# Performance work log

Measured on AMD Instinct MI355X. Metric: run time of the kernel, lower is better.

Reference implementation:

```python
import jax, jax.numpy as jnp
import numpy as np

B, T, D_IN, EMB, H = 2, 2048, 1024, 1024, 16
HD = EMB // H  # head_dim = 64


def setup_inputs() -> dict:
    key = jax.random.key(0)
    ks = jax.random.split(key, 3)
    scale_qkv = 1.0 / np.sqrt(D_IN)
    scale_o = 1.0 / np.sqrt(EMB)
    return {
        "x": jax.random.normal(ks[0], (B, T, D_IN), dtype=jnp.float32),
        "W_qkv": jax.random.normal(ks[1], (D_IN, 3 * EMB), dtype=jnp.float32) * scale_qkv,
        "b_qkv": jnp.zeros((3 * EMB,), dtype=jnp.float32),
        "W_o": jax.random.normal(ks[2], (EMB, EMB), dtype=jnp.float32) * scale_o,
        "b_o": jnp.zeros((EMB,), dtype=jnp.float32),
    }


def reference(x, W_qkv, b_qkv, W_o, b_o):
    b, t, _ = x.shape
    qkv = x @ W_qkv + b_qkv                      # [B,T,3*EMB]
    # Match torch: reshape to (B,T,H,3*HD) -> permute -> chunk into q,k,v
    qkv = qkv.reshape(b, t, H, 3 * HD).transpose(0, 2, 1, 3)  # [B,H,T,3*HD]
    q, k, v = jnp.split(qkv, 3, axis=-1)         # each [B,H,T,HD]
    scale = 1.0 / jnp.sqrt(jnp.asarray(HD, dtype=q.dtype))
    scores = jnp.einsum("bhqd,bhkd->bhqk", q, k) * scale  # [B,H,T,T]
    attn = jax.nn.softmax(scores, axis=-1)
    values = jnp.einsum("bhqk,bhkd->bhqd", attn, v)       # [B,H,T,HD]
    values = values.transpose(0, 2, 1, 3).reshape(b, t, EMB)
    return values @ W_o + b_o
```

## Files before the change

kernel.cpp:

```cpp
#include <hip/hip_runtime.h>
#include <math.h>

typedef __bf16 bf16x8 __attribute__((ext_vector_type(8)));
typedef float f32x4 __attribute__((ext_vector_type(4)));

#define GPTR(p) ((const __attribute__((address_space(1))) void*)(p))
#define LPTR(p) ((__attribute__((address_space(3))) void*)(p))

#define QSCALE 0.18033688011112042f

__device__ __forceinline__ unsigned short f2bf(float f) {
  unsigned int u = __float_as_uint(f);
  u += 0x7FFFu + ((u >> 16) & 1u);
  return (unsigned short)(u >> 16);
}

__device__ __forceinline__ unsigned int pack_bf2(float lo, float hi) {
  return __builtin_amdgcn_perm(__float_as_uint(hi) + 0x8000u,
                               __float_as_uint(lo) + 0x8000u, 0x07060302u);
}

__device__ __forceinline__ float fast_exp2(float x) {
#if __has_builtin(__builtin_amdgcn_exp2f)
  return __builtin_amdgcn_exp2f(x);
#else
  return exp2f(x);
#endif
}

__device__ __forceinline__ f32x4 zero4() {
  f32x4 z; z[0] = 0.f; z[1] = 0.f; z[2] = 0.f; z[3] = 0.f; return z;
}

__device__ __forceinline__ void permlane_swap32(unsigned int& a, unsigned int& b) {
  asm("v_permlane32_swap_b32 %0, %1" : "+v"(a), "+v"(b));
}
__device__ __forceinline__ void permlane_swap16(unsigned int& a, unsigned int& b) {
  asm("v_permlane16_swap_b32 %0, %1" : "+v"(a), "+v"(b));
}

__global__ void conv_x_bf16(const float* __restrict__ in, unsigned short* __restrict__ out) {
  int i = (blockIdx.x * 256 + threadIdx.x) * 4;
  float4 v = *(const float4*)(in + i);
  ushort4 o;
  o.x = f2bf(v.x); o.y = f2bf(v.y); o.z = f2bf(v.z); o.w = f2bf(v.w);
  *(ushort4*)(out + i) = o;
}

__global__ void transpose_conv(const float* __restrict__ in, unsigned short* __restrict__ out,
                               int K, int N) {
  __shared__ float tile[64][65];
  int k0 = blockIdx.y * 64, n0 = blockIdx.x * 64;
  int t = threadIdx.x;
#pragma unroll
  for (int p = 0; p < 16; ++p) {
    int l = p * 256 + t; int r = l >> 6, c = l & 63;
    tile[r][c] = in[(size_t)(k0 + r) * N + n0 + c];
  }
  __syncthreads();
#pragma unroll
  for (int p = 0; p < 16; ++p) {
    int l = p * 256 + t; int r = l >> 6, c = l & 63;
    out[(size_t)(n0 + r) * K + k0 + c] = f2bf(tile[c][r]);
  }
}

__global__ __launch_bounds__(256) void gemm_qkv(
    const unsigned short* __restrict__ A, const unsigned short* __restrict__ Bt,
    const float* __restrict__ bias,
    unsigned short* __restrict__ Qd, unsigned short* __restrict__ Kd,
    unsigned short* __restrict__ Vtd) {
  __shared__ unsigned short As[128 * 32];
  __shared__ unsigned short Bs[128 * 32];
  const int tid = threadIdx.x, wave = tid >> 6, lane = tid & 63;
  const int quad = lane >> 4, l16 = lane & 15;
  const int wm = (wave >> 1) * 64, wn = (wave & 1) * 64;
  const int m0 = blockIdx.y * 128, n0 = blockIdx.x * 128;
  f32x4 acc[4][4];
#pragma unroll
  for (int i = 0; i < 4; ++i)
#pragma unroll
    for (int j = 0; j < 4; ++j) acc[i][j] = zero4();

  const int c = wave * 64 + lane;
  const int rA = c >> 2, o16 = (c & 3) * 8;

  for (int k0 = 0; k0 < 1024; k0 += 32) {
    __syncthreads();
    __builtin_amdgcn_global_load_lds(GPTR(A + (size_t)(m0 + rA) * 1024 + k0 + o16),
                                     LPTR(As + wave * 512), 16, 0, 0);
    __builtin_amdgcn_global_load_lds(GPTR(A + (size_t)(m0 + 64 + rA) * 1024 + k0 + o16),
                                     LPTR(As + 2048 + wave * 512), 16, 0, 0);
    __builtin_amdgcn_global_load_lds(GPTR(Bt + (size_t)(n0 + rA) * 1024 + k0 + o16),
                                     LPTR(Bs + wave * 512), 16, 0, 0);
    __builtin_amdgcn_global_load_lds(GPTR(Bt + (size_t)(n0 + 64 + rA) * 1024 + k0 + o16),
                                     LPTR(Bs + 2048 + wave * 512), 16, 0, 0);
    __syncthreads();
    bf16x8 af[4], bfr[4];
#pragma unroll
    for (int mt = 0; mt < 4; ++mt)
      af[mt] = *(const bf16x8*)(As + (wm + mt * 16 + l16) * 32 + quad * 8);
#pragma unroll
    for (int nt = 0; nt < 4; ++nt)
      bfr[nt] = *(const bf16x8*)(Bs + (wn + nt * 16 + l16) * 32 + quad * 8);
#pragma unroll
    for (int mt = 0; mt < 4; ++mt)
#pragma unroll
      for (int nt = 0; nt < 4; ++nt)
        acc[mt][nt] = __builtin_amdgcn_mfma_f32_16x16x32_bf16(af[mt], bfr[nt], acc[mt][nt], 0, 0, 0);
  }

#pragma unroll
  for (int mt = 0; mt < 4; ++mt) {
#pragma unroll
    for (int nt = 0; nt < 4; ++nt) {
      int m = m0 + wm + mt * 16 + quad * 4;
      int n = n0 + wn + nt * 16 + l16;
      float bv = bias[n];
      int h = n / 192, rem = n - h * 192;
      int which = rem >> 6, d = rem & 63;
      int b = m >> 11, t0 = m & 2047;
      size_t head = (size_t)(b * 16 + h);
      f32x4 a = acc[mt][nt];
      if (which == 0) {
        size_t base = (head * 2048 + t0) * 64 + d;
#pragma unroll
        for (int i = 0; i < 4; ++i)
          Qd[base + (size_t)i * 64] = f2bf((a[i] + bv) * QSCALE);
      } else if (which == 1) {
        size_t base = head * 131072 + (size_t)(t0 >> 6) * 4096;
#pragma unroll
        for (int i = 0; i < 4; ++i) {
          int tt = t0 + i;
          Kd[base + (tt & 63) * 64 + (((d >> 3) ^ (tt & 7)) << 3) + (d & 7)] = f2bf(a[i] + bv);
        }
      } else {
        size_t base = head * 131072 + (size_t)(t0 >> 6) * 4096;
        ushort4 o;
        o.x = f2bf(a[0] + bv); o.y = f2bf(a[1] + bv);
        o.z = f2bf(a[2] + bv); o.w = f2bf(a[3] + bv);
        *(ushort4*)(Vtd + base + d * 64 + (((((t0 & 63) >> 3)) ^ (d & 7)) << 3) + (t0 & 7)) = o;
      }
    }
  }
}

__global__ __launch_bounds__(256) void flash_attn(
    const unsigned short* __restrict__ Qg,
    const unsigned short* __restrict__ Kg,
    const unsigned short* __restrict__ Vg,
    unsigned short* __restrict__ att) {
  __shared__ unsigned short Ks[2][4096];
  __shared__ unsigned short Vs[2][4096];
  const int tid = threadIdx.x, wave = tid >> 6, lane = tid & 63;
  const int quad = lane >> 4, l16 = lane & 15;
  const int h7 = l16 & 7;
  const int bh = blockIdx.y;
  const int q0 = blockIdx.x * 128 + wave * 32;

  bf16x8 bq[2][2];
#pragma unroll
  for (int qg = 0; qg < 2; ++qg)
#pragma unroll
    for (int kh = 0; kh < 2; ++kh)
      bq[qg][kh] = *(const bf16x8*)(Qg + ((size_t)bh * 2048 + q0 + qg * 16 + l16) * 64 + kh * 32 + quad * 8);

  f32x4 o[2][4];
#pragma unroll
  for (int qg = 0; qg < 2; ++qg)
#pragma unroll
    for (int i = 0; i < 4; ++i) o[qg][i] = zero4();
  float l_run[2] = {0.f, 0.f};

  const unsigned short* Kt = Kg + (size_t)bh * 131072 + lane * 8;
  const unsigned short* Vt = Vg + (size_t)bh * 131072 + lane * 8;
  const int so0 = wave * 512, so1 = (4 + wave) * 512;

#define STAGE_KV(buf, tile)                                                              \
  do {                                                                                   \
    const unsigned short* Kb_ = Kt + (tile) * 4096;                                      \
    const unsigned short* Vb_ = Vt + (tile) * 4096;                                      \
    __builtin_amdgcn_global_load_lds(GPTR(Kb_ + so0), LPTR(&Ks[buf][so0]), 16, 0, 0);    \
    __builtin_amdgcn_global_load_lds(GPTR(Kb_ + so1), LPTR(&Ks[buf][so1]), 16, 0, 0);    \
    __builtin_amdgcn_global_load_lds(GPTR(Vb_ + so0), LPTR(&Vs[buf][so0]), 16, 0, 0);    \
    __builtin_amdgcn_global_load_lds(GPTR(Vb_ + so1), LPTR(&Vs[buf][so1]), 16, 0, 0);    \
  } while (0)

  STAGE_KV(0, 0);
  __syncthreads();

  int cur = 0;
  for (int tile = 0; tile < 32; ++tile) {
    if (tile < 31) STAGE_KV(cur ^ 1, tile + 1);

    f32x4 s[2][4];
#pragma unroll
    for (int qg = 0; qg < 2; ++qg)
#pragma unroll
      for (int kt = 0; kt < 4; ++kt) s[qg][kt] = zero4();
#pragma unroll
    for (int kt = 0; kt < 4; ++kt) {
#pragma unroll
      for (int kh = 0; kh < 2; ++kh) {
        bf16x8 a = *(const bf16x8*)(&Ks[cur][(kt * 16 + l16) * 64 + (((kh * 4 + quad) ^ h7) << 3)]);
        s[0][kt] = __builtin_amdgcn_mfma_f32_16x16x32_bf16(a, bq[0][kh], s[0][kt], 0, 0, 0);
        s[1][kt] = __builtin_amdgcn_mfma_f32_16x16x32_bf16(a, bq[1][kh], s[1][kt], 0, 0, 0);
      }
    }

    unsigned int pw[2][4][2];
#pragma unroll
    for (int qg = 0; qg < 2; ++qg) {
      float lsum = 0.f;
      float pv[4][4];
#pragma unroll
      for (int kt = 0; kt < 4; ++kt)
#pragma unroll
        for (int r = 0; r < 4; ++r) {
          float p = fast_exp2(s[qg][kt][r]);
          pv[kt][r] = p;
          lsum += p;
        }
#pragma unroll
      for (int kt = 0; kt < 4; ++kt) {
        pw[qg][kt][0] = pack_bf2(pv[kt][0], pv[kt][1]);
        pw[qg][kt][1] = pack_bf2(pv[kt][2], pv[kt][3]);
      }
      lsum += __shfl_xor(lsum, 16);
      lsum += __shfl_xor(lsum, 32);
      l_run[qg] += lsum;
    }

    bf16x8 pf[2][2];
#pragma unroll
    for (int qg = 0; qg < 2; ++qg) {
#pragma unroll
      for (int st = 0; st < 2; ++st) {
        unsigned int a0 = pw[qg][2 * st][0], b0 = pw[qg][2 * st + 1][0];
        unsigned int a1 = pw[qg][2 * st][1], b1 = pw[qg][2 * st + 1][1];
        permlane_swap32(a0, b0); permlane_swap16(a0, b0);
        permlane_swap32(a1, b1); permlane_swap16(a1, b1);
        union { unsigned int u[4]; bf16x8 v; } x;
        x.u[0] = a0; x.u[1] = a1; x.u[2] = b0; x.u[3] = b1;
        pf[qg][st] = x.v;
      }
    }

#pragma unroll
    for (int st = 0; st < 2; ++st) {
#pragma unroll
      for (int mt = 0; mt < 4; ++mt) {
        bf16x8 av = *(const bf16x8*)(&Vs[cur][(mt * 16 + l16) * 64 + (((st * 4 + quad) ^ h7) << 3)]);
        o[0][mt] = __builtin_amdgcn_mfma_f32_16x16x32_bf16(av, pf[0][st], o[0][mt], 0, 0, 0);
        o[1][mt] = __builtin_amdgcn_mfma_f32_16x16x32_bf16(av, pf[1][st], o[1][mt], 0, 0, 0);
      }
    }

    __syncthreads();
    cur ^= 1;
  }
#undef STAGE_KV

  int b = bh >> 4, h = bh & 15;
#pragma unroll
  for (int qg = 0; qg < 2; ++qg) {
    float inv_l = 1.f / l_run[qg];
    unsigned short* orow = att + ((size_t)b * 2048 + q0 + qg * 16 + l16) * 1024 + h * 64;
#pragma unroll
    for (int mt = 0; mt < 4; ++mt) {
      ushort4 ov;
      ov.x = f2bf(o[qg][mt][0] * inv_l);
      ov.y = f2bf(o[qg][mt][1] * inv_l);
      ov.z = f2bf(o[qg][mt][2] * inv_l);
      ov.w = f2bf(o[qg][mt][3] * inv_l);
      *(ushort4*)(orow + mt * 16 + quad * 4) = ov;
    }
  }
}

__global__ __launch_bounds__(256) void gemm_out(
    const unsigned short* __restrict__ A, const unsigned short* __restrict__ Bt,
    const float* __restrict__ bias, float* __restrict__ out) {
  __shared__ unsigned short As[128 * 32];
  __shared__ unsigned short Bs[64 * 32];
  const int tid = threadIdx.x, wave = tid >> 6, lane = tid & 63;
  const int quad = lane >> 4, l16 = lane & 15;
  const int wm = (wave >> 1) * 64, wn = (wave & 1) * 32;
  const int m0 = blockIdx.y * 128, n0 = blockIdx.x * 64;
  f32x4 acc[4][2];
#pragma unroll
  for (int i = 0; i < 4; ++i)
#pragma unroll
    for (int j = 0; j < 2; ++j) acc[i][j] = zero4();

  const int c = wave * 64 + lane;
  const int rA = c >> 2, o16 = (c & 3) * 8;

  for (int k0 = 0; k0 < 1024; k0 += 32) {
    __syncthreads();
    __builtin_amdgcn_global_load_lds(GPTR(A + (size_t)(m0 + rA) * 1024 + k0 + o16),
                                     LPTR(As + wave * 512), 16, 0, 0);
    __builtin_amdgcn_global_load_lds(GPTR(A + (size_t)(m0 + 64 + rA) * 1024 + k0 + o16),
                                     LPTR(As + 2048 + wave * 512), 16, 0, 0);
    __builtin_amdgcn_global_load_lds(GPTR(Bt + (size_t)(n0 + rA) * 1024 + k0 + o16),
                                     LPTR(Bs + wave * 512), 16, 0, 0);
    __syncthreads();
    bf16x8 af[4], bfr[2];
#pragma unroll
    for (int mt = 0; mt < 4; ++mt)
      af[mt] = *(const bf16x8*)(As + (wm + mt * 16 + l16) * 32 + quad * 8);
#pragma unroll
    for (int nt = 0; nt < 2; ++nt)
      bfr[nt] = *(const bf16x8*)(Bs + (wn + nt * 16 + l16) * 32 + quad * 8);
#pragma unroll
    for (int mt = 0; mt < 4; ++mt)
#pragma unroll
      for (int nt = 0; nt < 2; ++nt)
        acc[mt][nt] = __builtin_amdgcn_mfma_f32_16x16x32_bf16(af[mt], bfr[nt], acc[mt][nt], 0, 0, 0);
  }

#pragma unroll
  for (int mt = 0; mt < 4; ++mt) {
#pragma unroll
    for (int nt = 0; nt < 2; ++nt) {
      int m = m0 + wm + mt * 16 + quad * 4;
      int n = n0 + wn + nt * 16 + l16;
      float bv = bias[n];
      float* orow = out + (size_t)m * 1024 + n;
      orow[0]        = acc[mt][nt][0] + bv;
      orow[1024]     = acc[mt][nt][1] + bv;
      orow[2 * 1024] = acc[mt][nt][2] + bv;
      orow[3 * 1024] = acc[mt][nt][3] + bv;
    }
  }
}

extern "C" void kernel_launch(void* const* d_in, const int* in_sizes, int n_in,
                              void* d_out, int out_size, void* d_ws, size_t ws_size,
                              hipStream_t stream) {
  const float* x    = (const float*)d_in[0];
  const float* Wqkv = (const float*)d_in[1];
  const float* bqkv = (const float*)d_in[2];
  const float* Wo   = (const float*)d_in[3];
  const float* bo   = (const float*)d_in[4];
  float* out = (float*)d_out;

  unsigned short* xb    = (unsigned short*)d_ws;
  unsigned short* wqkvt = xb    + (size_t)4096 * 1024;
  unsigned short* wot   = wqkvt + (size_t)3072 * 1024;
  unsigned short* Qd    = wot   + (size_t)1024 * 1024;
  unsigned short* Kd    = Qd    + (size_t)32 * 2048 * 64;
  unsigned short* Vtd   = Kd    + (size_t)32 * 2048 * 64;
  unsigned short* attb  = Vtd   + (size_t)32 * 2048 * 64;

  conv_x_bf16<<<4096, 256, 0, stream>>>(x, xb);
  transpose_conv<<<dim3(48, 16), 256, 0, stream>>>(Wqkv, wqkvt, 1024, 3072);
  transpose_conv<<<dim3(16, 16), 256, 0, stream>>>(Wo, wot, 1024, 1024);
  gemm_qkv<<<dim3(24, 32), 256, 0, stream>>>(xb, wqkvt, bqkv, Qd, Kd, Vtd);
  flash_attn<<<dim3(16, 32), 256, 0, stream>>>(Qd, Kd, Vtd, attb);
  gemm_out<<<dim3(16, 32), 256, 0, stream>>>(attb, wot, bo, out);
}
```

Before: 213.1 us.

## Double-buffer LDS tiles in QKV and output projection GEMMs

Both projection GEMMs now use two LDS buffers, issuing the async global-to-LDS loads for the next K slice before running the MFMAs on the current slice. The loop needs one barrier per iteration instead of two. The aim is to hide global load latency behind matrix math. It doubles LDS use per block, which may lower occupancy. The compiler's waitcnt handling for the async loads decides how much overlap is actually achieved.

```diff
diff --git a/kernel.cpp b/kernel.cpp
--- a/kernel.cpp
+++ b/kernel.cpp
@@ -70,8 +70,8 @@
     const float* __restrict__ bias,
     unsigned short* __restrict__ Qd, unsigned short* __restrict__ Kd,
     unsigned short* __restrict__ Vtd) {
-  __shared__ unsigned short As[128 * 32];
-  __shared__ unsigned short Bs[128 * 32];
+  __shared__ unsigned short As[2][4096];
+  __shared__ unsigned short Bs[2][4096];
   const int tid = threadIdx.x, wave = tid >> 6, lane = tid & 63;
   const int quad = lane >> 4, l16 = lane & 15;
   const int wm = (wave >> 1) * 64, wn = (wave & 1) * 64;
@@ -85,30 +85,39 @@
   const int c = wave * 64 + lane;
   const int rA = c >> 2, o16 = (c & 3) * 8;
 
+#define STAGEQ(B, K0)                                                                      \
+  do {                                                                                     \
+    __builtin_amdgcn_global_load_lds(GPTR(A + (size_t)(m0 + rA) * 1024 + (K0) + o16),      \
+                                     LPTR(&As[B][wave * 512]), 16, 0, 0);                  \
+    __builtin_amdgcn_global_load_lds(GPTR(A + (size_t)(m0 + 64 + rA) * 1024 + (K0) + o16), \
+                                     LPTR(&As[B][2048 + wave * 512]), 16, 0, 0);           \
+    __builtin_amdgcn_global_load_lds(GPTR(Bt + (size_t)(n0 + rA) * 1024 + (K0) + o16),     \
+                                     LPTR(&Bs[B][wave * 512]), 16, 0, 0);                  \
+    __builtin_amdgcn_global_load_lds(GPTR(Bt + (size_t)(n0 + 64 + rA) * 1024 + (K0) + o16),\
+                                     LPTR(&Bs[B][2048 + wave * 512]), 16, 0, 0);           \
+  } while (0)
+
+  STAGEQ(0, 0);
+  __syncthreads();
+  int cur = 0;
   for (int k0 = 0; k0 < 1024; k0 += 32) {
-    __syncthreads();
-    __builtin_amdgcn_global_load_lds(GPTR(A + (size_t)(m0 + rA) * 1024 + k0 + o16),
-                                     LPTR(As + wave * 512), 16, 0, 0);
-    __builtin_amdgcn_global_load_lds(GPTR(A + (size_t)(m0 + 64 + rA) * 1024 + k0 + o16),
-                                     LPTR(As + 2048 + wave * 512), 16, 0, 0);
-    __builtin_amdgcn_global_load_lds(GPTR(Bt + (size_t)(n0 + rA) * 1024 + k0 + o16),
-                                     LPTR(Bs + wave * 512), 16, 0, 0);
-    __builtin_amdgcn_global_load_lds(GPTR(Bt + (size_t)(n0 + 64 + rA) * 1024 + k0 + o16),
-                                     LPTR(Bs + 2048 + wave * 512), 16, 0, 0);
-    __syncthreads();
+    if (k0 < 992) STAGEQ(cur ^ 1, k0 + 32);
     bf16x8 af[4], bfr[4];
 #pragma unroll
     for (int mt = 0; mt < 4; ++mt)
-      af[mt] = *(const bf16x8*)(As + (wm + mt * 16 + l16) * 32 + quad * 8);
+      af[mt] = *(const bf16x8*)(&As[cur][(wm + mt * 16 + l16) * 32 + quad * 8]);
 #pragma unroll
     for (int nt = 0; nt < 4; ++nt)
-      bfr[nt] = *(const bf16x8*)(Bs + (wn + nt * 16 + l16) * 32 + quad * 8);
+      bfr[nt] = *(const bf16x8*)(&Bs[cur][(wn + nt * 16 + l16) * 32 + quad * 8]);
 #pragma unroll
     for (int mt = 0; mt < 4; ++mt)
 #pragma unroll
       for (int nt = 0; nt < 4; ++nt)
         acc[mt][nt] = __builtin_amdgcn_mfma_f32_16x16x32_bf16(af[mt], bfr[nt], acc[mt][nt], 0, 0, 0);
-  }
+    __syncthreads();
+    cur ^= 1;
+  }
+#undef STAGEQ
 
 #pragma unroll
   for (int mt = 0; mt < 4; ++mt) {
@@ -281,8 +290,8 @@
 __global__ __launch_bounds__(256) void gemm_out(
     const unsigned short* __restrict__ A, const unsigned short* __restrict__ Bt,
     const float* __restrict__ bias, float* __restrict__ out) {
-  __shared__ unsigned short As[128 * 32];
-  __shared__ unsigned short Bs[64 * 32];
+  __shared__ unsigned short As[2][4096];
+  __shared__ unsigned short Bs[2][2048];
   const int tid = threadIdx.x, wave = tid >> 6, lane = tid & 63;
   const int quad = lane >> 4, l16 = lane & 15;
   const int wm = (wave >> 1) * 64, wn = (wave & 1) * 32;
@@ -296,28 +305,37 @@
   const int c = wave * 64 + lane;
   const int rA = c >> 2, o16 = (c & 3) * 8;
 
+#define STAGEO(B, K0)                                                                      \
+  do {                                                                                     \
+    __builtin_amdgcn_global_load_lds(GPTR(A + (size_t)(m0 + rA) * 1024 + (K0) + o16),      \
+                                     LPTR(&As[B][wave * 512]), 16, 0, 0);                  \
+    __builtin_amdgcn_global_load_lds(GPTR(A + (size_t)(m0 + 64 + rA) * 1024 + (K0) + o16), \
+                                     LPTR(&As[B][2048 + wave * 512]), 16, 0, 0);           \
+    __builtin_amdgcn_global_load_lds(GPTR(Bt + (size_t)(n0 + rA) * 1024 + (K0) + o16),     \
+                                     LPTR(&Bs[B][wave * 512]), 16, 0, 0);                  \
+  } while (0)
+
+  STAGEO(0, 0);
+  __syncthreads();
+  int cur = 0;
   for (int k0 = 0; k0 < 1024; k0 += 32) {
-    __syncthreads();
-    __builtin_amdgcn_global_load_lds(GPTR(A + (size_t)(m0 + rA) * 1024 + k0 + o16),
-                                     LPTR(As + wave * 512), 16, 0, 0);
-    __builtin_amdgcn_global_load_lds(GPTR(A + (size_t)(m0 + 64 + rA) * 1024 + k0 + o16),
-                                     LPTR(As + 2048 + wave * 512), 16, 0, 0);
-    __builtin_amdgcn_global_load_lds(GPTR(Bt + (size_t)(n0 + rA) * 1024 + k0 + o16),
-                                     LPTR(Bs + wave * 512), 16, 0, 0);
-    __syncthreads();
+    if (k0 < 992) STAGEO(cur ^ 1, k0 + 32);
     bf16x8 af[4], bfr[2];
 #pragma unroll
     for (int mt = 0; mt < 4; ++mt)
-      af[mt] = *(const bf16x8*)(As + (wm + mt * 16 + l16) * 32 + quad * 8);
+      af[mt] = *(const bf16x8*)(&As[cur][(wm + mt * 16 + l16) * 32 + quad * 8]);
 #pragma unroll
     for (int nt = 0; nt < 2; ++nt)
-      bfr[nt] = *(const bf16x8*)(Bs + (wn + nt * 16 + l16) * 32 + quad * 8);
+      bfr[nt] = *(const bf16x8*)(&Bs[cur][(wn + nt * 16 + l16) * 32 + quad * 8]);
 #pragma unroll
     for (int mt = 0; mt < 4; ++mt)
 #pragma unroll
       for (int nt = 0; nt < 2; ++nt)
         acc[mt][nt] = __builtin_amdgcn_mfma_f32_16x16x32_bf16(af[mt], bfr[nt], acc[mt][nt], 0, 0, 0);
-  }
+    __syncthreads();
+    cur ^= 1;
+  }
+#undef STAGEO
 
 #pragma unroll
   for (int mt = 0; mt < 4; ++mt) {
```

Result: faster. 204.3 us (-4.1%).
